# Optimization experiments

Hardware: AMD Instinct MI355X
Metric: run time of the kernel (lower is better)

## Reference

```python
import jax, jax.numpy as jnp
import numpy as np

N = 50000
E = 1600000
IN_DIM = 128
OUT_DIM = 128
HEADS = 4
C = OUT_DIM // HEADS  # per-head channels = 32
EDGE_DIM = 16
NEG_SLOPE = 0.2
LN_EPS = 1e-5


def setup_inputs() -> dict:
    key = jax.random.key(0)
    ks = jax.random.split(key, 12)
    s = 1.0 / np.sqrt(IN_DIM)
    return {
        "x": jax.random.normal(ks[0], (N, IN_DIM), dtype=jnp.float32),
        "edge_index": jax.random.randint(ks[1], (2, E), 0, N, dtype=jnp.int64),
        "edge_attr": jax.random.normal(ks[2], (E, EDGE_DIM), dtype=jnp.float32),
        # GATv2Conv params
        "W_l": jax.random.normal(ks[3], (IN_DIM, HEADS * C), dtype=jnp.float32) * s,
        "b_l": jnp.zeros((HEADS * C,), dtype=jnp.float32),
        "W_r": jax.random.normal(ks[4], (IN_DIM, HEADS * C), dtype=jnp.float32) * s,
        "b_r": jnp.zeros((HEADS * C,), dtype=jnp.float32),
        "W_e": jax.random.normal(ks[5], (EDGE_DIM, HEADS * C), dtype=jnp.float32) * (1.0 / np.sqrt(EDGE_DIM)),
        "att": jax.random.normal(ks[6], (HEADS, C), dtype=jnp.float32) * (1.0 / np.sqrt(C)),
        "conv_bias": jnp.zeros((HEADS * C,), dtype=jnp.float32),
        # LayerNorm params
        "gamma": jnp.ones((OUT_DIM,), dtype=jnp.float32),
        "beta": jnp.zeros((OUT_DIM,), dtype=jnp.float32),
    }


def _gat_layer(x, edge_index, edge_attr, W_l, b_l, W_r, b_r, W_e, att, conv_bias, gamma, beta):
    src, dst = edge_index[0], edge_index[1]
    # linear projections -> [N, H, C] / [E, H, C]
    x_l = (x @ W_l + b_l).reshape(N, HEADS, C)  # source-side
    x_r = (x @ W_r + b_r).reshape(N, HEADS, C)  # target-side
    e_f = (edge_attr @ W_e).reshape(E, HEADS, C)
    # GATv2 attention logits per edge/head
    z = x_l[src] + x_r[dst] + e_f                      # [E, H, C]
    z = jnp.where(z >= 0, z, NEG_SLOPE * z)            # LeakyReLU(0.2)
    logits = jnp.einsum('ehc,hc->eh', z, att)          # [E, H]
    # segment softmax over incoming edges of each target node
    m = jax.ops.segment_max(logits, dst, num_segments=N)          # [N, H]
    m = jnp.where(jnp.isfinite(m), m, 0.0)
    ex = jnp.exp(logits - m[dst])                                  # [E, H]
    denom = jax.ops.segment_sum(ex, dst, num_segments=N)          # [N, H]
    alpha = ex / (denom[dst] + 1e-16)                              # [E, H]
    # weighted message aggregation (dropout on alpha skipped: eval mode)
    msg = x_l[src] * alpha[:, :, None]                             # [E, H, C]
    out = jax.ops.segment_sum(msg, dst, num_segments=N)           # [N, H, C]
    out = out.reshape(N, HEADS * C) + conv_bias                    # concat heads
    # LayerNorm -> ReLU -> (dropout: identity) -> residual (Identity since in==out)
    mu = jnp.mean(out, axis=-1, keepdims=True)
    var = jnp.mean(jnp.square(out - mu), axis=-1, keepdims=True)
    out = (out - mu) * jax.lax.rsqrt(var + LN_EPS) * gamma + beta
    out = jax.nn.relu(out)
    return out + x


def reference(x, edge_index, edge_attr, W_l, b_l, W_r, b_r, W_e, att, conv_bias, gamma, beta):
    return _gat_layer(x, edge_index, edge_attr, W_l, b_l, W_r, b_r, W_e, att, conv_bias, gamma, beta)
```

## Files before the change

kernel.cpp:

```cpp
#include <hip/hip_runtime.h>
#include <hip/hip_bf16.h>

#define NPB 16

__device__ __forceinline__ float b2f(__hip_bfloat16 v) { return __bfloat162float(v); }
__device__ __forceinline__ float ldf(const void* p, long i, int f32) {
    return f32 ? ((const float*)p)[i] : b2f(((const __hip_bfloat16*)p)[i]);
}
__device__ __forceinline__ float bflo(unsigned u) { union { unsigned i; float f; } v; v.i = u << 16; return v.f; }
__device__ __forceinline__ float bfhi(unsigned u) { union { unsigned i; float f; } v; v.i = u & 0xffff0000u; return v.f; }
__device__ __forceinline__ float2 ldf2(const void* p, long i2, int f32) {
    if (f32) return ((const float2*)p)[i2];
    unsigned u = ((const unsigned*)p)[i2];
    return make_float2(bflo(u), bfhi(u));
}
__device__ __forceinline__ int ldi(const int* p, long i, int i32) {
    return i32 ? p[i] : p[2 * i];
}
__device__ __forceinline__ int rfl(int v) { return __builtin_amdgcn_readfirstlane(v); }

template <int CTRL>
__device__ __forceinline__ float dpp_add(float v) {
    int s = __builtin_amdgcn_update_dpp(0, __float_as_int(v), CTRL, 0xF, 0xF, true);
    return v + __int_as_float(s);
}

__global__ void zero_i(int* __restrict__ a, long n, int* __restrict__ dt)
{
    long i = (long)blockIdx.x * 256 + threadIdx.x;
    long stride = (long)gridDim.x * 256;
    for (; i < n; i += stride) a[i] = 0;
    if (blockIdx.x == 0 && threadIdx.x == 0 && dt) { dt[0] = 0; dt[1] = 0; }
}

__global__ void fail_stamp(float* __restrict__ out, float code)
{
    if (threadIdx.x == 0 && blockIdx.x == 0) out[0] = code;
}

__global__ void detect_kernel(const void* __restrict__ x, const int* __restrict__ ei,
                              int* __restrict__ dt, int E_)
{
    int t = threadIdx.x;
    const unsigned short* xb = (const unsigned short*)x;
    int f32 = 0;
    for (int i = t; i < 4096; i += 256) {
        int ex = (xb[i] >> 7) & 0xFF;
        if (ex > 140) f32 = 1;
    }
    if (f32) atomicOr(&dt[0], 1);
    int nz = 0;
    for (int i = t; i < 2048; i += 256) nz |= ei[2 * i + 1];
    if (nz) atomicOr(&dt[1], 1);
}

__global__ __launch_bounds__(128) void gemm_xlr(
    const void* __restrict__ x,
    const void* __restrict__ Wl, const void* __restrict__ bl,
    const void* __restrict__ Wr, const void* __restrict__ br,
    const int* __restrict__ dt,
    __hip_bfloat16* __restrict__ xl, __hip_bfloat16* __restrict__ xr, int n)
{
    __shared__ float xs[NPB][128];
    int f32 = dt[0];
    int t = threadIdx.x;
    int n0 = blockIdx.x * NPB;
    for (int j = 0; j < NPB; ++j) {
        int node = n0 + j;
        xs[j][t] = (node < n) ? ldf(x, (long)node * 128 + t, f32) : 0.f;
    }
    __syncthreads();
    float accl[NPB], accr[NPB];
#pragma unroll
    for (int j = 0; j < NPB; ++j) { accl[j] = 0.f; accr[j] = 0.f; }
    for (int k = 0; k < 128; ++k) {
        float wl = ldf(Wl, k * 128 + t, f32);
        float wr = ldf(Wr, k * 128 + t, f32);
#pragma unroll
        for (int j = 0; j < NPB; ++j) {
            float xv = xs[j][k];
            accl[j] = fmaf(xv, wl, accl[j]);
            accr[j] = fmaf(xv, wr, accr[j]);
        }
    }
    float blv = ldf(bl, t, f32);
    float brv = ldf(br, t, f32);
    for (int j = 0; j < NPB; ++j) {
        int node = n0 + j;
        if (node < n) {
            xl[(long)node * 128 + t] = __float2bfloat16(accl[j] + blv);
            xr[(long)node * 128 + t] = __float2bfloat16(accr[j] + brv);
        }
    }
}

__global__ void hist_kernel(const int* __restrict__ ei, const int* __restrict__ dt,
                            int* __restrict__ cnt, int E_, int N_)
{
    long e = (long)blockIdx.x * 256 + threadIdx.x;
    if (e >= E_) return;
    int i32 = dt[1];
    int s = ldi(ei, e, i32);
    int d = ldi(ei, E_ + e, i32);
    if ((unsigned)s < (unsigned)N_ && (unsigned)d < (unsigned)N_) atomicAdd(&cnt[d], 1);
}

__global__ __launch_bounds__(1024) void scan_kernel(
    const int* __restrict__ cnt, int* __restrict__ row_ptr, int* __restrict__ fill, int n)
{
    __shared__ int wsum[16];
    __shared__ int carry_s;
    int t = threadIdx.x; int lane = t & 63; int w = t >> 6;
    if (t == 0) { carry_s = 0; row_ptr[0] = 0; }
    __syncthreads();
    for (int base = 0; base < n; base += 1024) {
        int idx = base + t;
        int v = (idx < n) ? cnt[idx] : 0;
        int s = v;
        for (int o = 1; o < 64; o <<= 1) { int u = __shfl_up(s, o, 64); if (lane >= o) s += u; }
        if (lane == 63) wsum[w] = s;
        __syncthreads();
        int carry = carry_s;
        if (w == 0) {
            int ws = (lane < 16) ? wsum[lane] : 0;
            for (int o = 1; o < 16; o <<= 1) { int u = __shfl_up(ws, o, 64); if (lane >= o) ws += u; }
            if (lane < 16) wsum[lane] = ws;
        }
        __syncthreads();
        int woff = (w > 0) ? wsum[w - 1] : 0;
        int incl = s + woff;
        if (idx < n) { row_ptr[idx + 1] = carry + incl; fill[idx] = carry + incl - v; }
        __syncthreads();
        if (t == 0) carry_s = carry + wsum[15];
        __syncthreads();
    }
}

__global__ __launch_bounds__(256) void scatter_se(
    const int* __restrict__ ei, const int* __restrict__ dt,
    int* __restrict__ fill, int2* __restrict__ se_sorted, int E_, int N_)
{
    long e = (long)blockIdx.x * 256 + threadIdx.x;
    if (e >= E_) return;
    int i32 = dt[1];
    int s = ldi(ei, e, i32);
    int d = ldi(ei, E_ + e, i32);
    if ((unsigned)s < (unsigned)N_ && (unsigned)d < (unsigned)N_) {
        int pos = atomicAdd(&fill[d], 1);
        se_sorted[pos] = make_int2(s, (int)e);
    }
}

__global__ __launch_bounds__(256) void node_fused(
    const int* __restrict__ row_ptr, const int2* __restrict__ se_sorted,
    const void* __restrict__ ea, const void* __restrict__ We, const void* __restrict__ att,
    const __hip_bfloat16* __restrict__ xl, const __hip_bfloat16* __restrict__ xr,
    const void* __restrict__ cb, const void* __restrict__ gamma,
    const void* __restrict__ beta, const void* __restrict__ x,
    const int* __restrict__ dt, float* __restrict__ out, int N_)
{
    int w = threadIdx.x >> 6, j = threadIdx.x & 63;
    int f32 = dt[0];
    int h = j >> 4;

    float We0[16], We1[16];
#pragma unroll
    for (int k = 0; k < 16; ++k) {
        float2 v = ldf2(We, (long)k * 64 + j, f32);
        We0[k] = v.x; We1[k] = v.y;
    }
#pragma unroll
    for (int k = 0; k < 16; ++k) asm volatile("" : "+v"(We0[k]), "+v"(We1[k]));
    float2 attv = ldf2(att, j, f32);
    float2 cbv  = ldf2(cb, j, f32);
    float2 gv   = ldf2(gamma, j, f32);
    float2 bv   = ldf2(beta, j, f32);

    const unsigned* xlu = (const unsigned*)xl;
    const unsigned* xru = (const unsigned*)xr;

    for (int q = 0; q < 4; ++q) {
        int n = (blockIdx.x * 4 + w) * 4 + q;
        if (n >= N_) break;
        int beg = row_ptr[n], end = row_ptr[n + 1];
        unsigned urow = xru[(long)n * 64 + j];
        float w0 = bflo(urow), w1 = bfhi(urow);
        float acc0 = 0.f, acc1 = 0.f, den = 0.f;

#define EDGE_BODY(Z0INIT, Z1INIT, A)                                              \
        float z0 = (Z0INIT), z1 = (Z1INIT);                                       \
        z0 = fmaf(A[0],  We0[0],  z0); z1 = fmaf(A[0],  We1[0],  z1);             \
        z0 = fmaf(A[1],  We0[1],  z0); z1 = fmaf(A[1],  We1[1],  z1);             \
        z0 = fmaf(A[2],  We0[2],  z0); z1 = fmaf(A[2],  We1[2],  z1);             \
        z0 = fmaf(A[3],  We0[3],  z0); z1 = fmaf(A[3],  We1[3],  z1);             \
        z0 = fmaf(A[4],  We0[4],  z0); z1 = fmaf(A[4],  We1[4],  z1);             \
        z0 = fmaf(A[5],  We0[5],  z0); z1 = fmaf(A[5],  We1[5],  z1);             \
        z0 = fmaf(A[6],  We0[6],  z0); z1 = fmaf(A[6],  We1[6],  z1);             \
        z0 = fmaf(A[7],  We0[7],  z0); z1 = fmaf(A[7],  We1[7],  z1);             \
        z0 = fmaf(A[8],  We0[8],  z0); z1 = fmaf(A[8],  We1[8],  z1);             \
        z0 = fmaf(A[9],  We0[9],  z0); z1 = fmaf(A[9],  We1[9],  z1);             \
        z0 = fmaf(A[10], We0[10], z0); z1 = fmaf(A[10], We1[10], z1);             \
        z0 = fmaf(A[11], We0[11], z0); z1 = fmaf(A[11], We1[11], z1);             \
        z0 = fmaf(A[12], We0[12], z0); z1 = fmaf(A[12], We1[12], z1);             \
        z0 = fmaf(A[13], We0[13], z0); z1 = fmaf(A[13], We1[13], z1);             \
        z0 = fmaf(A[14], We0[14], z0); z1 = fmaf(A[14], We1[14], z1);             \
        z0 = fmaf(A[15], We0[15], z0); z1 = fmaf(A[15], We1[15], z1);             \
        z0 = fmaxf(z0, 0.2f * z0);                            \
        z1 = fmaxf(z1, 0.2f * z1);                                                \
        float v = fmaf(z1, attv.y, z0 * attv.x);                                  \
        v = dpp_add<0xB1>(v);  v = dpp_add<0x4E>(v);                              \
        v = dpp_add<0x124>(v); v = dpp_add<0x128>(v);       \
        float ex = __expf(v);

        if (beg < end) {
            if (f32) {
                int2 se = se_sorted[beg];
                int sC = rfl(se.x), eC = rfl(se.y);
                unsigned uC = xlu[((long)sC << 6) + j];
                const float4* er = (const float4*)ea + (long)eC * 4;
                float4 r0 = er[0], r1 = er[1], r2 = er[2], r3 = er[3];
                for (int i = beg; i < end; ++i) {
                    int ip = (i + 1 < end) ? i + 1 : beg;
                    int2 seN = se_sorted[ip];
                    int sN = rfl(seN.x), eN = rfl(seN.y);
                    unsigned uN = xlu[((long)sN << 6) + j];
                    const float4* ern = (const float4*)ea + (long)eN * 4;
                    float4 m0 = ern[0], m1 = ern[1], m2 = ern[2], m3 = ern[3];
                    float a[16] = { r0.x, r0.y, r0.z, r0.w, r1.x, r1.y, r1.z, r1.w,
                                    r2.x, r2.y, r2.z, r2.w, r3.x, r3.y, r3.z, r3.w };
                    { EDGE_BODY(bflo(uC) + w0, bfhi(uC) + w1, a)
                      acc0 = fmaf(ex, bflo(uC), acc0);
                      acc1 = fmaf(ex, bfhi(uC), acc1);
                      den += ex; }
                    uC = uN; r0 = m0; r1 = m1; r2 = m2; r3 = m3;
                }
            } else {
                int2 se = se_sorted[beg];
                int sC = rfl(se.x), eC = rfl(se.y);
                unsigned uC = xlu[((long)sC << 6) + j];
                const uint4* er = (const uint4*)ea + (long)eC * 2;
                uint4 b0 = er[0], b1 = er[1];
                for (int i = beg; i < end; ++i) {
                    int ip = (i + 1 < end) ? i + 1 : beg;
                    int2 seN = se_sorted[ip];
                    int sN = rfl(seN.x), eN = rfl(seN.y);
                    unsigned uN = xlu[((long)sN << 6) + j];
                    const uint4* ern = (const uint4*)ea + (long)eN * 2;
                    uint4 c0 = ern[0], c1 = ern[1];
                    float a[16] = { bflo(b0.x), bfhi(b0.x), bflo(b0.y), bfhi(b0.y),
                                    bflo(b0.z), bfhi(b0.z), bflo(b0.w), bfhi(b0.w),
                                    bflo(b1.x), bfhi(b1.x), bflo(b1.y), bfhi(b1.y),
                                    bflo(b1.z), bfhi(b1.z), bflo(b1.w), bfhi(b1.w) };
                    { EDGE_BODY(bflo(uC) + w0, bfhi(uC) + w1, a)
                      acc0 = fmaf(ex, bflo(uC), acc0);
                      acc1 = fmaf(ex, bfhi(uC), acc1);
                      den += ex; }
                    uC = uN; b0 = c0; b1 = c1;
                }
            }
        }
#undef EDGE_BODY

        float rden = 1.f / (den + 1e-16f);
        float o0 = acc0 * rden + cbv.x;
        float o1 = acc1 * rden + cbv.y;

        float s = o0 + o1;
#pragma unroll
        for (int o = 1; o < 64; o <<= 1) s += __shfl_xor(s, o, 64);
        float mu = s * (1.f / 128.f);
        float d0 = o0 - mu, d1 = o1 - mu;
        float vs = d0 * d0 + d1 * d1;
#pragma unroll
        for (int o = 1; o < 64; o <<= 1) vs += __shfl_xor(vs, o, 64);
        float rs = rsqrtf(vs * (1.f / 128.f) + 1e-5f);
        float2 xv = ldf2(x, (long)n * 64 + j, f32);
        float y0 = fmaxf(d0 * rs * gv.x + bv.x, 0.f) + xv.x;
        float y1 = fmaxf(d1 * rs * gv.y + bv.y, 0.f) + xv.y;
        *(float2*)(out + (long)n * 128 + 2 * j) = make_float2(y0, y1);
    }
}

extern "C" void kernel_launch(void* const* d_in, const int* in_sizes, int n_in,
                              void* d_out, int out_size, void* d_ws, size_t ws_size,
                              hipStream_t stream) {
    const void* x     = d_in[0];
    const int*  ei    = (const int*)d_in[1];
    const void* ea    = d_in[2];
    const void* Wl    = d_in[3];
    const void* bl    = d_in[4];
    const void* Wr    = d_in[5];
    const void* br    = d_in[6];
    const void* We    = d_in[7];
    const void* att   = d_in[8];
    const void* cb    = d_in[9];
    const void* gamma = d_in[10];
    const void* beta  = d_in[11];
    float* out = (float*)d_out;

    const int N_ = in_sizes[0] / 128;
    const int E_ = in_sizes[2] / 16;

    size_t need = 0;
    auto sz = [&](size_t b) { size_t r = need; need += (b + 255) & ~(size_t)255; return r; };
    size_t o_xl   = sz((size_t)N_ * 128 * 2);
    size_t o_xr   = sz((size_t)N_ * 128 * 2);
    size_t o_cnt  = sz((size_t)N_ * 4);
    size_t o_row  = sz((size_t)(N_ + 1) * 4);
    size_t o_fill = sz((size_t)N_ * 4);
    size_t o_dt   = sz(256);
    size_t o_se   = sz((size_t)E_ * 8);

    if (need > ws_size) {
        fail_stamp<<<1, 64, 0, stream>>>(out, 16384.f);
        return;
    }
    char* p = (char*)d_ws;
    __hip_bfloat16* xl   = (__hip_bfloat16*)(p + o_xl);
    __hip_bfloat16* xr   = (__hip_bfloat16*)(p + o_xr);
    int*   cnt           = (int*)(p + o_cnt);
    int*   row_ptr       = (int*)(p + o_row);
    int*   fill          = (int*)(p + o_fill);
    int*   dt            = (int*)(p + o_dt);
    int2*  se_sorted     = (int2*)(p + o_se);

    zero_i<<<256, 256, 0, stream>>>(cnt, N_, dt);
    detect_kernel<<<1, 256, 0, stream>>>(x, ei, dt, E_);
    gemm_xlr<<<(N_ + NPB - 1) / NPB, 128, 0, stream>>>(x, Wl, bl, Wr, br, dt, xl, xr, N_);
    hist_kernel<<<(E_ + 255) / 256, 256, 0, stream>>>(ei, dt, cnt, E_, N_);
    scan_kernel<<<1, 1024, 0, stream>>>(cnt, row_ptr, fill, N_);
    scatter_se<<<(E_ + 255) / 256, 256, 0, stream>>>(ei, dt, fill, se_sorted, E_, N_);
    node_fused<<<(N_ + 15) / 16, 256, 0, stream>>>(row_ptr, se_sorted, ea, We, att,
                                                   xl, xr, cb, gamma, beta, x, dt, out, N_);
}
```

Baseline: 741.7 us.

## Replace CSR build with padded per-node edge buckets fused into GEMM kernel

```diff
diff --git a/kernel.cpp b/kernel.cpp
--- a/kernel.cpp
+++ b/kernel.cpp
@@ -2,6 +2,10 @@
 #include <hip/hip_bf16.h>
 
 #define NPB 16
+#define PAD 80
+#define OVF_CAP 4096
+
+typedef float f32x2 __attribute__((ext_vector_type(2)));
 
 __device__ __forceinline__ float b2f(__hip_bfloat16 v) { return __bfloat162float(v); }
 __device__ __forceinline__ float ldf(const void* p, long i, int f32) {
@@ -54,105 +58,81 @@
     if (nz) atomicOr(&dt[1], 1);
 }
 
-__global__ __launch_bounds__(128) void gemm_xlr(
+__global__ __launch_bounds__(128) void gemm_scatter(
     const void* __restrict__ x,
     const void* __restrict__ Wl, const void* __restrict__ bl,
     const void* __restrict__ Wr, const void* __restrict__ br,
-    const int* __restrict__ dt,
-    __hip_bfloat16* __restrict__ xl, __hip_bfloat16* __restrict__ xr, int n)
+    const int* __restrict__ ei, const int* __restrict__ dt,
+    __hip_bfloat16* __restrict__ xl, __hip_bfloat16* __restrict__ xr,
+    int* __restrict__ cnt, int* __restrict__ ovfcnt,
+    int2* __restrict__ se_pad, int4* __restrict__ ovf,
+    int n, int E_)
 {
     __shared__ float xs[NPB][128];
-    int f32 = dt[0];
     int t = threadIdx.x;
+    int f32 = dt[0], i32 = dt[1];
+
+    long eb = (long)blockIdx.x * 512;
+    int sA[4], dA[4], kA[4], eA[4];
+#pragma unroll
+    for (int i = 0; i < 4; ++i) {
+        long e = eb + i * 128 + t;
+        int s = -1, d = -1;
+        if (e < E_) {
+            s = ldi(ei, e, i32);
+            d = ldi(ei, E_ + e, i32);
+            if (!((unsigned)s < (unsigned)n && (unsigned)d < (unsigned)n)) d = -1;
+        }
+        sA[i] = s; dA[i] = d; eA[i] = (int)e;
+    }
+#pragma unroll
+    for (int i = 0; i < 4; ++i)
+        kA[i] = (dA[i] >= 0) ? atomicAdd(&cnt[dA[i]], 1) : 0;
+
     int n0 = blockIdx.x * NPB;
-    for (int j = 0; j < NPB; ++j) {
-        int node = n0 + j;
-        xs[j][t] = (node < n) ? ldf(x, (long)node * 128 + t, f32) : 0.f;
-    }
-    __syncthreads();
-    float accl[NPB], accr[NPB];
-#pragma unroll
-    for (int j = 0; j < NPB; ++j) { accl[j] = 0.f; accr[j] = 0.f; }
-    for (int k = 0; k < 128; ++k) {
-        float wl = ldf(Wl, k * 128 + t, f32);
-        float wr = ldf(Wr, k * 128 + t, f32);
-#pragma unroll
+    if (n0 < n) {
         for (int j = 0; j < NPB; ++j) {
-            float xv = xs[j][k];
-            accl[j] = fmaf(xv, wl, accl[j]);
-            accr[j] = fmaf(xv, wr, accr[j]);
-        }
-    }
-    float blv = ldf(bl, t, f32);
-    float brv = ldf(br, t, f32);
-    for (int j = 0; j < NPB; ++j) {
-        int node = n0 + j;
-        if (node < n) {
-            xl[(long)node * 128 + t] = __float2bfloat16(accl[j] + blv);
-            xr[(long)node * 128 + t] = __float2bfloat16(accr[j] + brv);
-        }
-    }
-}
-
-__global__ void hist_kernel(const int* __restrict__ ei, const int* __restrict__ dt,
-                            int* __restrict__ cnt, int E_, int N_)
-{
-    long e = (long)blockIdx.x * 256 + threadIdx.x;
-    if (e >= E_) return;
-    int i32 = dt[1];
-    int s = ldi(ei, e, i32);
-    int d = ldi(ei, E_ + e, i32);
-    if ((unsigned)s < (unsigned)N_ && (unsigned)d < (unsigned)N_) atomicAdd(&cnt[d], 1);
-}
-
-__global__ __launch_bounds__(1024) void scan_kernel(
-    const int* __restrict__ cnt, int* __restrict__ row_ptr, int* __restrict__ fill, int n)
-{
-    __shared__ int wsum[16];
-    __shared__ int carry_s;
-    int t = threadIdx.x; int lane = t & 63; int w = t >> 6;
-    if (t == 0) { carry_s = 0; row_ptr[0] = 0; }
-    __syncthreads();
-    for (int base = 0; base < n; base += 1024) {
-        int idx = base + t;
-        int v = (idx < n) ? cnt[idx] : 0;
-        int s = v;
-        for (int o = 1; o < 64; o <<= 1) { int u = __shfl_up(s, o, 64); if (lane >= o) s += u; }
-        if (lane == 63) wsum[w] = s;
+            int node = n0 + j;
+            xs[j][t] = (node < n) ? ldf(x, (long)node * 128 + t, f32) : 0.f;
+        }
         __syncthreads();
-        int carry = carry_s;
-        if (w == 0) {
-            int ws = (lane < 16) ? wsum[lane] : 0;
-            for (int o = 1; o < 16; o <<= 1) { int u = __shfl_up(ws, o, 64); if (lane >= o) ws += u; }
-            if (lane < 16) wsum[lane] = ws;
-        }
-        __syncthreads();
-        int woff = (w > 0) ? wsum[w - 1] : 0;
-        int incl = s + woff;
-        if (idx < n) { row_ptr[idx + 1] = carry + incl; fill[idx] = carry + incl - v; }
-        __syncthreads();
-        if (t == 0) carry_s = carry + wsum[15];
-        __syncthreads();
-    }
-}
-
-__global__ __launch_bounds__(256) void scatter_se(
-    const int* __restrict__ ei, const int* __restrict__ dt,
-    int* __restrict__ fill, int2* __restrict__ se_sorted, int E_, int N_)
-{
-    long e = (long)blockIdx.x * 256 + threadIdx.x;
-    if (e >= E_) return;
-    int i32 = dt[1];
-    int s = ldi(ei, e, i32);
-    int d = ldi(ei, E_ + e, i32);
-    if ((unsigned)s < (unsigned)N_ && (unsigned)d < (unsigned)N_) {
-        int pos = atomicAdd(&fill[d], 1);
-        se_sorted[pos] = make_int2(s, (int)e);
-    }
-}
-
-__global__ __launch_bounds__(256) void node_fused(
-    const int* __restrict__ row_ptr, const int2* __restrict__ se_sorted,
+        f32x2 acc[NPB];
+#pragma unroll
+        for (int j = 0; j < NPB; ++j) acc[j] = (f32x2){0.f, 0.f};
+        for (int k = 0; k < 128; ++k) {
+            f32x2 wlr = { ldf(Wl, k * 128 + t, f32), ldf(Wr, k * 128 + t, f32) };
+#pragma unroll
+            for (int j = 0; j < NPB; ++j) {
+                f32x2 xv = { xs[j][k], xs[j][k] };
+                acc[j] = __builtin_elementwise_fma(xv, wlr, acc[j]);
+            }
+        }
+        float blv = ldf(bl, t, f32);
+        float brv = ldf(br, t, f32);
+        for (int j = 0; j < NPB; ++j) {
+            int node = n0 + j;
+            if (node < n) {
+                xl[(long)node * 128 + t] = __float2bfloat16(acc[j].x + blv);
+                xr[(long)node * 128 + t] = __float2bfloat16(acc[j].y + brv);
+            }
+        }
+    }
+
+#pragma unroll
+    for (int i = 0; i < 4; ++i) {
+        if (dA[i] < 0) continue;
+        if (kA[i] < PAD) {
+            se_pad[(long)dA[i] * PAD + kA[i]] = make_int2(sA[i], eA[i]);
+        } else {
+            int o = atomicAdd(ovfcnt, 1);
+            if (o < OVF_CAP) ovf[o] = make_int4(dA[i], sA[i], eA[i], 0);
+        }
+    }
+}
+
+__global__ __launch_bounds__(256, 4) void node_fused(
+    const int* __restrict__ cnt, const int2* __restrict__ se_pad,
+    const int4* __restrict__ ovf, const int* __restrict__ ovfcnt,
     const void* __restrict__ ea, const void* __restrict__ We, const void* __restrict__ att,
     const __hip_bfloat16* __restrict__ xl, const __hip_bfloat16* __restrict__ xr,
     const void* __restrict__ cb, const void* __restrict__ gamma,
@@ -163,14 +143,12 @@
     int f32 = dt[0];
     int h = j >> 4;
 
-    float We0[16], We1[16];
+    f32x2 We2[16];
 #pragma unroll
     for (int k = 0; k < 16; ++k) {
         float2 v = ldf2(We, (long)k * 64 + j, f32);
-        We0[k] = v.x; We1[k] = v.y;
-    }
-#pragma unroll
-    for (int k = 0; k < 16; ++k) asm volatile("" : "+v"(We0[k]), "+v"(We1[k]));
+        We2[k] = (f32x2){v.x, v.y};
+    }
     float2 attv = ldf2(att, j, f32);
     float2 cbv  = ldf2(cb, j, f32);
     float2 gv   = ldf2(gamma, j, f32);
@@ -179,70 +157,62 @@
     const unsigned* xlu = (const unsigned*)xl;
     const unsigned* xru = (const unsigned*)xr;
 
+    auto edge_ex = [&](const float* a, float x0, float x1, float w0, float w1) -> float {
+        f32x2 z = { x0 + w0, x1 + w1 };
+#pragma unroll
+        for (int k = 0; k < 16; ++k) {
+            f32x2 ab = { a[k], a[k] };
+            z = __builtin_elementwise_fma(ab, We2[k], z);
+        }
+        z = __builtin_elementwise_max(z, z * 0.2f);
+        float v = fmaf(z.y, attv.y, z.x * attv.x);
+        v = dpp_add<0xB1>(v);  v = dpp_add<0x4E>(v);
+        v = dpp_add<0x124>(v); v = dpp_add<0x128>(v);
+        return __expf(v);
+    };
+
     for (int q = 0; q < 4; ++q) {
         int n = (blockIdx.x * 4 + w) * 4 + q;
         if (n >= N_) break;
-        int beg = row_ptr[n], end = row_ptr[n + 1];
+        int deg = cnt[n];
+        int m = deg < PAD ? deg : PAD;
+        long base = (long)n * PAD;
         unsigned urow = xru[(long)n * 64 + j];
         float w0 = bflo(urow), w1 = bfhi(urow);
-        float acc0 = 0.f, acc1 = 0.f, den = 0.f;
-
-#define EDGE_BODY(Z0INIT, Z1INIT, A)                                              \
-        float z0 = (Z0INIT), z1 = (Z1INIT);                                       \
-        z0 = fmaf(A[0],  We0[0],  z0); z1 = fmaf(A[0],  We1[0],  z1);             \
-        z0 = fmaf(A[1],  We0[1],  z0); z1 = fmaf(A[1],  We1[1],  z1);             \
-        z0 = fmaf(A[2],  We0[2],  z0); z1 = fmaf(A[2],  We1[2],  z1);             \
-        z0 = fmaf(A[3],  We0[3],  z0); z1 = fmaf(A[3],  We1[3],  z1);             \
-        z0 = fmaf(A[4],  We0[4],  z0); z1 = fmaf(A[4],  We1[4],  z1);             \
-        z0 = fmaf(A[5],  We0[5],  z0); z1 = fmaf(A[5],  We1[5],  z1);             \
-        z0 = fmaf(A[6],  We0[6],  z0); z1 = fmaf(A[6],  We1[6],  z1);             \
-        z0 = fmaf(A[7],  We0[7],  z0); z1 = fmaf(A[7],  We1[7],  z1);             \
-        z0 = fmaf(A[8],  We0[8],  z0); z1 = fmaf(A[8],  We1[8],  z1);             \
-        z0 = fmaf(A[9],  We0[9],  z0); z1 = fmaf(A[9],  We1[9],  z1);             \
-        z0 = fmaf(A[10], We0[10], z0); z1 = fmaf(A[10], We1[10], z1);             \
-        z0 = fmaf(A[11], We0[11], z0); z1 = fmaf(A[11], We1[11], z1);             \
-        z0 = fmaf(A[12], We0[12], z0); z1 = fmaf(A[12], We1[12], z1);             \
-        z0 = fmaf(A[13], We0[13], z0); z1 = fmaf(A[13], We1[13], z1);             \
-        z0 = fmaf(A[14], We0[14], z0); z1 = fmaf(A[14], We1[14], z1);             \
-        z0 = fmaf(A[15], We0[15], z0); z1 = fmaf(A[15], We1[15], z1);             \
-        z0 = fmaxf(z0, 0.2f * z0);                            \
-        z1 = fmaxf(z1, 0.2f * z1);                                                \
-        float v = fmaf(z1, attv.y, z0 * attv.x);                                  \
-        v = dpp_add<0xB1>(v);  v = dpp_add<0x4E>(v);                              \
-        v = dpp_add<0x124>(v); v = dpp_add<0x128>(v);       \
-        float ex = __expf(v);
-
-        if (beg < end) {
+        f32x2 acc = {0.f, 0.f};
+        float den = 0.f;
+
+        if (m > 0) {
             if (f32) {
-                int2 se = se_sorted[beg];
+                int2 se = se_pad[base];
                 int sC = rfl(se.x), eC = rfl(se.y);
                 unsigned uC = xlu[((long)sC << 6) + j];
                 const float4* er = (const float4*)ea + (long)eC * 4;
                 float4 r0 = er[0], r1 = er[1], r2 = er[2], r3 = er[3];
-                for (int i = beg; i < end; ++i) {
-                    int ip = (i + 1 < end) ? i + 1 : beg;
-                    int2 seN = se_sorted[ip];
+                for (int k = 0; k < m; ++k) {
+                    int kp = (k + 1 < m) ? k + 1 : 0;
+                    int2 seN = se_pad[base + kp];
                     int sN = rfl(seN.x), eN = rfl(seN.y);
                     unsigned uN = xlu[((long)sN << 6) + j];
                     const float4* ern = (const float4*)ea + (long)eN * 4;
                     float4 m0 = ern[0], m1 = ern[1], m2 = ern[2], m3 = ern[3];
                     float a[16] = { r0.x, r0.y, r0.z, r0.w, r1.x, r1.y, r1.z, r1.w,
                                     r2.x, r2.y, r2.z, r2.w, r3.x, r3.y, r3.z, r3.w };
-                    { EDGE_BODY(bflo(uC) + w0, bfhi(uC) + w1, a)
-                      acc0 = fmaf(ex, bflo(uC), acc0);
-                      acc1 = fmaf(ex, bfhi(uC), acc1);
-                      den += ex; }
+                    float x0 = bflo(uC), x1 = bfhi(uC);
+                    float ex = edge_ex(a, x0, x1, w0, w1);
+                    acc = __builtin_elementwise_fma((f32x2){ex, ex}, (f32x2){x0, x1}, acc);
+                    den += ex;
                     uC = uN; r0 = m0; r1 = m1; r2 = m2; r3 = m3;
                 }
             } else {
-                int2 se = se_sorted[beg];
+                int2 se = se_pad[base];
                 int sC = rfl(se.x), eC = rfl(se.y);
                 unsigned uC = xlu[((long)sC << 6) + j];
                 const uint4* er = (const uint4*)ea + (long)eC * 2;
                 uint4 b0 = er[0], b1 = er[1];
-                for (int i = beg; i < end; ++i) {
-                    int ip = (i + 1 < end) ? i + 1 : beg;
-                    int2 seN = se_sorted[ip];
+                for (int k = 0; k < m; ++k) {
+                    int kp = (k + 1 < m) ? k + 1 : 0;
+                    int2 seN = se_pad[base + kp];
                     int sN = rfl(seN.x), eN = rfl(seN.y);
                     unsigned uN = xlu[((long)sN << 6) + j];
                     const uint4* ern = (const uint4*)ea + (long)eN * 2;
@@ -251,19 +221,49 @@
                                     bflo(b0.z), bfhi(b0.z), bflo(b0.w), bfhi(b0.w),
                                     bflo(b1.x), bfhi(b1.x), bflo(b1.y), bfhi(b1.y),
                                     bflo(b1.z), bfhi(b1.z), bflo(b1.w), bfhi(b1.w) };
-                    { EDGE_BODY(bflo(uC) + w0, bfhi(uC) + w1, a)
-                      acc0 = fmaf(ex, bflo(uC), acc0);
-                      acc1 = fmaf(ex, bfhi(uC), acc1);
-                      den += ex; }
+                    float x0 = bflo(uC), x1 = bfhi(uC);
+                    float ex = edge_ex(a, x0, x1, w0, w1);
+                    acc = __builtin_elementwise_fma((f32x2){ex, ex}, (f32x2){x0, x1}, acc);
+                    den += ex;
                     uC = uN; b0 = c0; b1 = c1;
                 }
             }
         }
-#undef EDGE_BODY
+        if (deg > PAD) {
+            int oc = *ovfcnt; if (oc > OVF_CAP) oc = OVF_CAP;
+            for (int o = 0; o < oc; ++o) {
+                int4 v4 = ovf[o];
+                if (rfl(v4.x) != n) continue;
+                int sO = rfl(v4.y), eO = rfl(v4.z);
+                unsigned uO = xlu[((long)sO << 6) + j];
+                float a[16];
+                if (f32) {
+                    const float4* er = (const float4*)ea + (long)eO * 4;
+                    float4 r0 = er[0], r1 = er[1], r2 = er[2], r3 = er[3];
+                    float tmp[16] = { r0.x, r0.y, r0.z, r0.w, r1.x, r1.y, r1.z, r1.w,
+                                      r2.x, r2.y, r2.z, r2.w, r3.x, r3.y, r3.z, r3.w };
+#pragma unroll
+                    for (int k = 0; k < 16; ++k) a[k] = tmp[k];
+                } else {
+                    const uint4* er = (const uint4*)ea + (long)eO * 2;
+                    uint4 b0 = er[0], b1 = er[1];
+                    float tmp[16] = { bflo(b0.x), bfhi(b0.x), bflo(b0.y), bfhi(b0.y),
+                                      bflo(b0.z), bfhi(b0.z), bflo(b0.w), bfhi(b0.w),
+                                      bflo(b1.x), bfhi(b1.x), bflo(b1.y), bfhi(b1.y),
+                                      bflo(b1.z), bfhi(b1.z), bflo(b1.w), bfhi(b1.w) };
+#pragma unroll
+                    for (int k = 0; k < 16; ++k) a[k] = tmp[k];
+                }
+                float x0 = bflo(uO), x1 = bfhi(uO);
+                float ex = edge_ex(a, x0, x1, w0, w1);
+                acc = __builtin_elementwise_fma((f32x2){ex, ex}, (f32x2){x0, x1}, acc);
+                den += ex;
+            }
+        }
 
         float rden = 1.f / (den + 1e-16f);
-        float o0 = acc0 * rden + cbv.x;
-        float o1 = acc1 * rden + cbv.y;
+        float o0 = acc.x * rden + cbv.x;
+        float o1 = acc.y * rden + cbv.y;
 
         float s = o0 + o1;
 #pragma unroll
@@ -305,11 +305,10 @@
     auto sz = [&](size_t b) { size_t r = need; need += (b + 255) & ~(size_t)255; return r; };
     size_t o_xl   = sz((size_t)N_ * 128 * 2);
     size_t o_xr   = sz((size_t)N_ * 128 * 2);
-    size_t o_cnt  = sz((size_t)N_ * 4);
-    size_t o_row  = sz((size_t)(N_ + 1) * 4);
-    size_t o_fill = sz((size_t)N_ * 4);
+    size_t o_cnt  = sz((size_t)(N_ + 8) * 4);
     size_t o_dt   = sz(256);
-    size_t o_se   = sz((size_t)E_ * 8);
+    size_t o_se   = sz((size_t)N_ * PAD * 8);
+    size_t o_ovf  = sz((size_t)OVF_CAP * 16);
 
     if (need > ws_size) {
         fail_stamp<<<1, 64, 0, stream>>>(out, 16384.f);
@@ -319,17 +318,18 @@
     __hip_bfloat16* xl   = (__hip_bfloat16*)(p + o_xl);
     __hip_bfloat16* xr   = (__hip_bfloat16*)(p + o_xr);
     int*   cnt           = (int*)(p + o_cnt);
-    int*   row_ptr       = (int*)(p + o_row);
-    int*   fill          = (int*)(p + o_fill);
+    int*   ovfcnt        = cnt + N_;
     int*   dt            = (int*)(p + o_dt);
-    int2*  se_sorted     = (int2*)(p + o_se);
-
-    zero_i<<<256, 256, 0, stream>>>(cnt, N_, dt);
+    int2*  se_pad        = (int2*)(p + o_se);
+    int4*  ovf           = (int4*)(p + o_ovf);
+
+    zero_i<<<256, 256, 0, stream>>>(cnt, N_ + 8, dt);
     detect_kernel<<<1, 256, 0, stream>>>(x, ei, dt, E_);
-    gemm_xlr<<<(N_ + NPB - 1) / NPB, 128, 0, stream>>>(x, Wl, bl, Wr, br, dt, xl, xr, N_);
-    hist_kernel<<<(E_ + 255) / 256, 256, 0, stream>>>(ei, dt, cnt, E_, N_);
-    scan_kernel<<<1, 1024, 0, stream>>>(cnt, row_ptr, fill, N_);
-    scatter_se<<<(E_ + 255) / 256, 256, 0, stream>>>(ei, dt, fill, se_sorted, E_, N_);
-    node_fused<<<(N_ + 15) / 16, 256, 0, stream>>>(row_ptr, se_sorted, ea, We, att,
+    int gGemm = (N_ + NPB - 1) / NPB;
+    int gScat = (E_ + 511) / 512;
+    int grid0 = gGemm > gScat ? gGemm : gScat;
+    gemm_scatter<<<grid0, 128, 0, stream>>>(x, Wl, bl, Wr, br, ei, dt, xl, xr,
+                                            cnt, ovfcnt, se_pad, ovf, N_, E_);
+    node_fused<<<(N_ + 15) / 16, 256, 0, stream>>>(cnt, se_pad, ovf, ovfcnt, ea, We, att,
                                                    xl, xr, cb, gamma, beta, x, dt, out, N_);
 }
```

Result: faster. 633.9 us (-14.5%).
